# Kernel tuning notes

Measured on AMD Instinct MI355X. Metric: run time of the kernel, lower is better.

Reference implementation:

```python
import jax, jax.numpy as jnp
import numpy as np

H = 32        # query heads
KV = 8        # kv heads
HD = 128      # head_dim
EPS = 1e-6
THETA = 1e6
T = 2048
D = 4096


def _rms_norm(x, w):
    # x: [T, heads, HD]
    var = jnp.mean(jnp.square(x), axis=-1, keepdims=True)
    return x * jax.lax.rsqrt(var + EPS) * w


def _rope(x, cos, sin):
    # NEOX-style rotary: split last dim in halves. x: [T, heads, HD]
    x1, x2 = jnp.split(x, 2, axis=-1)
    return jnp.concatenate([x1 * cos - x2 * sin, x2 * cos + x1 * sin], axis=-1)


def setup_inputs() -> dict:
    key = jax.random.key(0)
    k1, k2, k3 = jax.random.split(key, 3)
    s = 1.0 / np.sqrt(D)
    return {
        "positions": jnp.arange(T, dtype=jnp.int32),
        "hidden_states": jax.random.normal(k1, (T, D), dtype=jnp.float32),
        "w_qkv": jax.random.normal(k2, (D, (H + 2 * KV) * HD), dtype=jnp.float32) * s,
        "q_norm_w": jnp.ones((HD,), dtype=jnp.float32),
        "k_norm_w": jnp.ones((HD,), dtype=jnp.float32),
        "w_o": jax.random.normal(k3, (H * HD, D), dtype=jnp.float32) * s,
    }


def reference(positions, hidden_states, w_qkv, q_norm_w, k_norm_w, w_o):
    scale = HD ** -0.5
    qkv = hidden_states @ w_qkv                              # [T, (H+2KV)*HD]
    q = qkv[:, : H * HD].reshape(T, H, HD)
    k = qkv[:, H * HD : (H + KV) * HD].reshape(T, KV, HD)
    v = qkv[:, (H + KV) * HD :].reshape(T, KV, HD)

    # per-head RMSNorm on q/k (Qwen3 QK-norm)
    q = _rms_norm(q, q_norm_w)
    k = _rms_norm(k, k_norm_w)

    # RoPE
    inv_freq = 1.0 / (THETA ** (jnp.arange(0, HD, 2, dtype=jnp.float32) / HD))
    freqs = positions.astype(jnp.float32)[:, None] * inv_freq  # [T, HD/2]
    cos = jnp.cos(freqs)[:, None, :]                            # [T, 1, HD/2]
    sin = jnp.sin(freqs)[:, None, :]
    q = _rope(q, cos, sin)
    k = _rope(k, cos, sin)

    # GQA: repeat kv heads
    rep = H // KV
    k = jnp.repeat(k, rep, axis=1)                           # [T, H, HD]
    v = jnp.repeat(v, rep, axis=1)

    # causal SDPA
    scores = jnp.einsum("thd,shd->hts", q, k) * scale        # [H, T, T]
    causal = jnp.tril(jnp.ones((T, T), dtype=bool))
    scores = jnp.where(causal[None], scores, jnp.finfo(scores.dtype).min)
    probs = jax.nn.softmax(scores, axis=-1)
    attn = jnp.einsum("hts,shd->thd", probs, v).reshape(T, H * HD)

    return attn @ w_o                                        # [T, D]
```

## Files before the change

### kernel.cpp

```cpp
#include <hip/hip_runtime.h>

#define TT   2048
#define DD   4096
#define NH   32
#define NKVH 8
#define HDM  128
#define KD   4096
#define NQKV 6144

typedef unsigned short u16;
typedef short v8s __attribute__((ext_vector_type(8)));
typedef float v4f __attribute__((ext_vector_type(4)));

#define QSCALE 0.12751744547734565f
#define EOFF   17.312340490667562f

__device__ __forceinline__ u16 f2bf(float f) {
    unsigned u = __builtin_bit_cast(unsigned, f);
    u += 0x7fffu + ((u >> 16) & 1u);
    return (u16)(u >> 16);
}
__device__ __forceinline__ float bf2f(u16 h) {
    return __builtin_bit_cast(float, ((unsigned)h) << 16);
}
__device__ __forceinline__ void gl2lds16(const void* g, void* l) {
    using gv = const __attribute__((address_space(1))) void;
    using lv = __attribute__((address_space(3))) void;
    __builtin_amdgcn_global_load_lds((gv*)g, (lv*)l, 16, 0, 0);
}

__device__ __forceinline__ void transpose_tile64(const float* __restrict__ in,
                                                 u16* __restrict__ out,
                                                 int K, int N, int n0, int k0,
                                                 float* tile, int t) {
    int rc = t >> 4, cc = (t & 15) * 4;
#pragma unroll
    for (int p = 0; p < 4; ++p) {
        int k = p * 16 + rc;
        float4 v = *(const float4*)&in[(size_t)(k0 + k) * N + n0 + cc];
        tile[k * 65 + cc] = v.x; tile[k * 65 + cc + 1] = v.y;
        tile[k * 65 + cc + 2] = v.z; tile[k * 65 + cc + 3] = v.w;
    }
    __syncthreads();
    int rn = t >> 3, ck = (t & 7) * 8;
#pragma unroll
    for (int p = 0; p < 2; ++p) {
        int n = p * 32 + rn;
        v8s tv;
#pragma unroll
        for (int j = 0; j < 8; ++j) tv[j] = (short)f2bf(tile[(ck + j) * 65 + n]);
        *(v8s*)&out[(size_t)(n0 + n) * K + k0 + ck] = tv;
    }
}

__global__ __launch_bounds__(256) void prep_all_kernel(const float* __restrict__ hidden,
                                                       u16* __restrict__ hid_bf,
                                                       const int* __restrict__ positions,
                                                       float* __restrict__ cosT,
                                                       float* __restrict__ sinT,
                                                       const float* __restrict__ w_qkv,
                                                       u16* __restrict__ wqkv_t) {
    __shared__ float tile[64 * 65];
    int b = blockIdx.x;
    if (b < 4096) {
        size_t i = ((size_t)b * 256 + threadIdx.x) * 8;
        float4 a = *(const float4*)&hidden[i];
        float4 c = *(const float4*)&hidden[i + 4];
        v8s tv;
        tv[0] = (short)f2bf(a.x); tv[1] = (short)f2bf(a.y);
        tv[2] = (short)f2bf(a.z); tv[3] = (short)f2bf(a.w);
        tv[4] = (short)f2bf(c.x); tv[5] = (short)f2bf(c.y);
        tv[6] = (short)f2bf(c.z); tv[7] = (short)f2bf(c.w);
        *(v8s*)&hid_bf[i] = tv;
    } else if (b < 4608) {
        int idx = (b - 4096) * 256 + threadIdx.x;
        int tp = idx >> 6, i = idx & 63;
        float invf = exp2f(-(float)i * 0.31143075889569023f);
        float f = (float)positions[tp] * invf;
        cosT[idx] = cosf(f);
        sinT[idx] = sinf(f);
    } else {
        int bx = b - 4608;
        int n0 = (bx % 96) * 64, k0 = (bx / 96) * 64;
        transpose_tile64(w_qkv, wqkv_t, 4096, NQKV, n0, k0, tile, threadIdx.x);
    }
}

__global__ __launch_bounds__(256) void gemm_bt_kernel(
    const u16* __restrict__ A, const u16* __restrict__ Bt, float* __restrict__ C, int N)
{
    __shared__ __align__(16) u16 smem[16896];
    u16* As = smem;
    u16* Bs = smem + 8192;
    int tid = threadIdx.x;
    int wave = tid >> 6, lane = tid & 63;
    int quad = lane >> 4, l15 = lane & 15;
    int lm = l15 & 7;
    int wm = wave >> 1, wn = wave & 1;
    int m0 = blockIdx.y * 128, n0 = blockIdx.x * 128;

    v4f acc[4][4];
    v4f z4 = {0.f, 0.f, 0.f, 0.f};
#pragma unroll
    for (int mi = 0; mi < 4; ++mi)
#pragma unroll
        for (int ni = 0; ni < 4; ++ni) acc[mi][ni] = z4;

    int rsub = lane >> 3;
    int cg = (lane & 7) ^ rsub;
    const u16* Ag = &A[(size_t)m0 * KD + cg * 8];
    const u16* Bg = &Bt[(size_t)n0 * KD + cg * 8];

    for (int k0 = 0; k0 < KD; k0 += 64) {
        __syncthreads();
#pragma unroll
        for (int c = 0; c < 4; ++c) {
            int ch = wave * 4 + c;
            int row = ch * 8 + rsub;
            gl2lds16(&Ag[(size_t)row * KD + k0], &As[ch * 512]);
            gl2lds16(&Bg[(size_t)row * KD + k0], &Bs[ch * 512]);
        }
        __syncthreads();
#pragma unroll
        for (int ks = 0; ks < 2; ++ks) {
            v8s af[4], bfr[4];
#pragma unroll
            for (int mi = 0; mi < 4; ++mi) {
                int ar = wm * 64 + mi * 16 + l15;
                af[mi] = *(const v8s*)&As[ar * 64 + ((((ks << 2) + quad) ^ lm) << 3)];
            }
#pragma unroll
            for (int ni = 0; ni < 4; ++ni) {
                int br = wn * 64 + ni * 16 + l15;
                bfr[ni] = *(const v8s*)&Bs[br * 64 + ((((ks << 2) + quad) ^ lm) << 3)];
            }
#pragma unroll
            for (int mi = 0; mi < 4; ++mi)
#pragma unroll
                for (int ni = 0; ni < 4; ++ni)
                    acc[mi][ni] = __builtin_amdgcn_mfma_f32_16x16x32_bf16(
                        af[mi], bfr[ni], acc[mi][ni], 0, 0, 0);
        }
    }
#pragma unroll
    for (int mi = 0; mi < 4; ++mi)
#pragma unroll
        for (int ni = 0; ni < 4; ++ni)
#pragma unroll
            for (int r = 0; r < 4; ++r)
                C[(size_t)(m0 + wm * 64 + mi * 16 + quad * 4 + r) * N +
                  (n0 + wn * 64 + ni * 16 + l15)] = acc[mi][ni][r];
}

__global__ __launch_bounds__(512, 2) void gemm256_qkv_kernel(
    const u16* __restrict__ A, const u16* __restrict__ Bt,
    const float* __restrict__ qw, const float* __restrict__ kw,
    const float* __restrict__ cosT, const float* __restrict__ sinT,
    u16* __restrict__ Qb, u16* __restrict__ Kb, u16* __restrict__ Vt)
{
    __shared__ __align__(16) char smem_raw[131072];
    u16* lds = (u16*)smem_raw;
    const int tid = threadIdx.x;
    const int wave = tid >> 6, lane = tid & 63;
    const int quad = lane >> 4, l15 = lane & 15, lm = l15 & 7;
    const int wm = wave >> 2, wn = wave & 3;
    const int m0 = blockIdx.y * 256, n0 = blockIdx.x * 256;

    v4f acc[2][2][4][2];
    v4f z4 = {0.f, 0.f, 0.f, 0.f};
#pragma unroll
    for (int a0 = 0; a0 < 2; ++a0)
#pragma unroll
        for (int b0 = 0; b0 < 2; ++b0)
#pragma unroll
            for (int mi = 0; mi < 4; ++mi)
#pragma unroll
                for (int ni = 0; ni < 2; ++ni) acc[a0][b0][mi][ni] = z4;

    const int rsub = lane >> 3;
    const int cg = (lane & 7) ^ rsub;
    const u16* Ag = &A[(size_t)m0 * KD + cg * 8];
    const u16* Bg = &Bt[(size_t)n0 * KD + cg * 8];
    const int ch0 = wave * 2;
    const int g0 = (quad ^ lm) << 3;
    const int g1 = ((4 + quad) ^ lm) << 3;

#define STAGE_A(tt, h) do { \
    int _b = ((tt) & 1) * 32768; \
    gl2lds16(&Ag[(size_t)((h) * 128 + (ch0 + 0) * 8 + rsub) * KD + (size_t)(tt) * 64], \
             &lds[_b + (h) * 8192 + (ch0 + 0) * 512]); \
    gl2lds16(&Ag[(size_t)((h) * 128 + (ch0 + 1) * 8 + rsub) * KD + (size_t)(tt) * 64], \
             &lds[_b + (h) * 8192 + (ch0 + 1) * 512]); \
  } while (0)
#define STAGE_B(tt, h) do { \
    int _b = ((tt) & 1) * 32768 + 16384; \
    gl2lds16(&Bg[(size_t)((h) * 128 + (ch0 + 0) * 8 + rsub) * KD + (size_t)(tt) * 64], \
             &lds[_b + (h) * 8192 + (ch0 + 0) * 512]); \
    gl2lds16(&Bg[(size_t)((h) * 128 + (ch0 + 1) * 8 + rsub) * KD + (size_t)(tt) * 64], \
             &lds[_b + (h) * 8192 + (ch0 + 1) * 512]); \
  } while (0)

    v8s af[4][2], bfr[2][2];

#define PHASE(QM, QN, RDA, RDB, STAGE_CODE, WAIT_CODE) do { \
    if (RDA) { \
      _Pragma("unroll") \
      for (int mi = 0; mi < 4; ++mi) { \
        const u16* ap = &lds[bo + ((QM) * 128 + wm * 64 + mi * 16 + l15) * 64]; \
        af[mi][0] = *(const v8s*)&ap[g0]; \
        af[mi][1] = *(const v8s*)&ap[g1]; \
      } } \
    if (RDB) { \
      _Pragma("unroll") \
      for (int ni = 0; ni < 2; ++ni) { \
        const u16* bp = &lds[bo + 16384 + ((QN) * 128 + wn * 32 + ni * 16 + l15) * 64]; \
        bfr[ni][0] = *(const v8s*)&bp[g0]; \
        bfr[ni][1] = *(const v8s*)&bp[g1]; \
      } } \
    STAGE_CODE; \
    __builtin_amdgcn_s_barrier(); \
    asm volatile("s_waitcnt lgkmcnt(0)" ::: "memory"); \
    __builtin_amdgcn_sched_barrier(0); \
    __builtin_amdgcn_s_setprio(1); \
    _Pragma("unroll") \
    for (int mi = 0; mi < 4; ++mi) \
      _Pragma("unroll") \
      for (int ni = 0; ni < 2; ++ni) { \
        acc[QM][QN][mi][ni] = __builtin_amdgcn_mfma_f32_16x16x32_bf16( \
            af[mi][0], bfr[ni][0], acc[QM][QN][mi][ni], 0, 0, 0); \
        acc[QM][QN][mi][ni] = __builtin_amdgcn_mfma_f32_16x16x32_bf16( \
            af[mi][1], bfr[ni][1], acc[QM][QN][mi][ni], 0, 0, 0); \
      } \
    __builtin_amdgcn_s_setprio(0); \
    WAIT_CODE; \
    __builtin_amdgcn_s_barrier(); \
  } while (0)

    STAGE_A(0, 0); STAGE_B(0, 0); STAGE_B(0, 1); STAGE_A(0, 1);
    STAGE_A(1, 0); STAGE_B(1, 1); STAGE_A(1, 1);
    asm volatile("s_waitcnt vmcnt(6)" ::: "memory");
    __builtin_amdgcn_s_barrier();

#pragma unroll 2
    for (int t = 0; t < 64; ++t) {
        const int bo = (t & 1) * 32768;
        PHASE(0, 0, 1, 1, { if (t + 1 < 64) STAGE_B(t + 1, 0); }, {});
        PHASE(0, 1, 0, 1, { if (t + 2 < 64) STAGE_A(t + 2, 0); }, {});
        PHASE(1, 1, 1, 0, { if (t + 2 < 64) STAGE_B(t + 2, 1); }, {});
        PHASE(1, 0, 0, 1, { if (t + 2 < 64) STAGE_A(t + 2, 1); },
              { if (t + 2 < 64) { asm volatile("s_waitcnt vmcnt(6)" ::: "memory"); }
                else            { asm volatile("s_waitcnt vmcnt(0)" ::: "memory"); } });
    }
#undef PHASE
#undef STAGE_A
#undef STAGE_B

    u16* Ct = lds;
    const int t0q = blockIdx.y * 256;
#pragma unroll
    for (int hh = 0; hh < 2; ++hh) {
        __syncthreads();
#pragma unroll
        for (int qm = 0; qm < 2; ++qm)
#pragma unroll
            for (int mi = 0; mi < 4; ++mi)
#pragma unroll
                for (int ni = 0; ni < 2; ++ni)
#pragma unroll
                    for (int r = 0; r < 4; ++r)
                        Ct[(qm * 128 + wm * 64 + mi * 16 + quad * 4 + r) * 132 +
                           wn * 32 + ni * 16 + l15] = f2bf(acc[qm][hh][mi][ni][r]);
        __syncthreads();
        const int head = blockIdx.x * 2 + hh;
        if (head < 40) {
            if (tid < 256) {
                const int row = tid;
                const float* w = (head < 32) ? qw : kw;
                float ss = 0.f;
                for (int i = 0; i < 128; ++i) {
                    float x = bf2f(Ct[row * 132 + i]);
                    ss += x * x;
                }
                float rs = rsqrtf(ss * (1.0f / 128.0f) + 1e-6f);
                if (head < 32) rs *= QSCALE;
                const int ti = t0q + row;
                for (int i = 0; i < 64; ++i) {
                    float x1 = bf2f(Ct[row * 132 + i]) * rs * w[i];
                    float x2 = bf2f(Ct[row * 132 + 64 + i]) * rs * w[64 + i];
                    float c = cosT[ti * 64 + i], s = sinT[ti * 64 + i];
                    Ct[row * 132 + i]      = f2bf(x1 * c - x2 * s);
                    Ct[row * 132 + 64 + i] = f2bf(x2 * c + x1 * s);
                }
            }
            __syncthreads();
            u16* dst = (head < 32) ? &Qb[((size_t)head * TT + t0q) * HDM]
                                   : &Kb[((size_t)(head - 32) * TT + t0q) * HDM];
            for (int cix = tid; cix < 256 * 16; cix += 512) {
                int row = cix >> 4, part = (cix & 15) * 8;
                v8s tv;
#pragma unroll
                for (int j = 0; j < 8; ++j) tv[j] = (short)Ct[row * 132 + part + j];
                *(v8s*)&dst[row * HDM + part] = tv;
            }
        } else {
            const int kvh = head - 40;
            if (tid < 128) {
                const int hd = tid;
                for (int tb = 0; tb < 32; ++tb) {
                    v8s tv;
#pragma unroll
                    for (int j = 0; j < 8; ++j) tv[j] = (short)Ct[(tb * 8 + j) * 132 + hd];
                    *(v8s*)&Vt[((size_t)kvh * HDM + hd) * TT + t0q + tb * 8] = tv;
                }
            }
        }
    }
}

__global__ __launch_bounds__(256) void attn_plus_kernel(
    const u16* __restrict__ Qb, const u16* __restrict__ Kb,
    const u16* __restrict__ Vt, u16* __restrict__ Ob,
    const float* __restrict__ w_o, u16* __restrict__ wo_t)
{
    __shared__ __align__(16) char smem_raw[40960];
    int tid = threadIdx.x;
    if (blockIdx.x >= 1024) {
        int bx = blockIdx.x - 1024;
        int n0 = (bx & 63) * 64, k0 = (bx >> 6) * 64;
        transpose_tile64(w_o, wo_t, 4096, 4096, n0, k0, (float*)smem_raw, tid);
        return;
    }
    u16* Kl = (u16*)smem_raw;
    u16* Vl = (u16*)(smem_raw + 16384);
    u16* Pl = (u16*)(smem_raw + 32768);
    int wave = tid >> 6, lane = tid & 63;
    int quad = lane >> 4, l15 = lane & 15;
    int idx = blockIdx.x;
    int h = idx & 31;
    int qb = 31 - (idx >> 5);
    int kv = h >> 2;
    int q0 = qb * 64;
    int lm = l15 & 7;

    v8s qf[4];
    {
        const u16* qr = &Qb[((size_t)h * TT + q0 + wave * 16 + l15) * HDM];
#pragma unroll
        for (int ks = 0; ks < 4; ++ks) qf[ks] = *(const v8s*)&qr[ks * 32 + quad * 8];
    }

    v4f z4 = {0.f, 0.f, 0.f, 0.f};
    v4f of[8];
#pragma unroll
    for (int i = 0; i < 8; ++i) of[i] = z4;
    float lsum[4];
#pragma unroll
    for (int r = 0; r < 4; ++r) lsum[r] = 0.f;
    u16* Pw = &Pl[wave * 1024];

    for (int s0 = 0; s0 <= q0; s0 += 64) {
        __syncthreads();
#pragma unroll
        for (int c = 0; c < 4; ++c) {
            int ch = wave * 4 + c;
            int rk = ch * 4 + (lane >> 4);
            int ck = (lane & 15) ^ (rk & 7);
            gl2lds16(&Kb[((size_t)kv * TT + s0 + rk) * HDM + ck * 8], &Kl[ch * 512]);
            int rv = ch * 8 + (lane >> 3);
            int cv = (lane & 7) ^ (rv & 7);
            gl2lds16(&Vt[((size_t)kv * HDM + rv) * TT + s0 + cv * 8], &Vl[ch * 512]);
        }
        __syncthreads();
        v4f sf[4];
#pragma unroll
        for (int nt = 0; nt < 4; ++nt) {
            v4f cacc = z4;
#pragma unroll
            for (int ks = 0; ks < 4; ++ks)
                cacc = __builtin_amdgcn_mfma_f32_16x16x32_bf16(
                    qf[ks],
                    *(const v8s*)&Kl[(nt * 16 + l15) * 128 + (((ks * 4 + quad) ^ lm) << 3)],
                    cacc, 0, 0, 0);
            sf[nt] = cacc;
        }
        if (s0 == q0) {
#pragma unroll
            for (int nt = 0; nt < 4; ++nt) {
                int sg = s0 + nt * 16 + l15;
#pragma unroll
                for (int r = 0; r < 4; ++r) {
                    int qg = q0 + wave * 16 + quad * 4 + r;
                    if (sg > qg) sf[nt][r] = -3.0e38f;
                }
            }
        }
#pragma unroll
        for (int nt = 0; nt < 4; ++nt)
#pragma unroll
            for (int r = 0; r < 4; ++r) {
                float p = exp2f(sf[nt][r] - EOFF);
                sf[nt][r] = p;
                lsum[r] += p;
            }
#pragma unroll
        for (int nt = 0; nt < 4; ++nt)
#pragma unroll
            for (int r = 0; r < 4; ++r) {
                int row = quad * 4 + r;
                int pch = ((nt << 1) + (l15 >> 3)) ^ (row & 7);
                Pw[row * 64 + pch * 8 + (l15 & 7)] = f2bf(sf[nt][r]);
            }
#pragma unroll
        for (int sub = 0; sub < 2; ++sub) {
            v8s pa = *(const v8s*)&Pw[l15 * 64 + ((((sub << 2) + quad) ^ lm) << 3)];
#pragma unroll
            for (int nt = 0; nt < 8; ++nt)
                of[nt] = __builtin_amdgcn_mfma_f32_16x16x32_bf16(
                    pa,
                    *(const v8s*)&Vl[(nt * 16 + l15) * 64 + ((((sub << 2) + quad) ^ lm) << 3)],
                    of[nt], 0, 0, 0);
        }
    }
#pragma unroll
    for (int off = 1; off < 16; off <<= 1)
#pragma unroll
        for (int r = 0; r < 4; ++r) lsum[r] += __shfl_xor(lsum[r], off, 64);
    float invl[4];
#pragma unroll
    for (int r = 0; r < 4; ++r) invl[r] = 1.0f / lsum[r];
#pragma unroll
    for (int nt = 0; nt < 8; ++nt)
#pragma unroll
        for (int r = 0; r < 4; ++r)
            Ob[(size_t)(q0 + wave * 16 + quad * 4 + r) * (NH * HDM) + h * HDM + nt * 16 + l15] =
                f2bf(of[nt][r] * invl[r]);
}

extern "C" void kernel_launch(void* const* d_in, const int* in_sizes, int n_in,
                              void* d_out, int out_size, void* d_ws, size_t ws_size,
                              hipStream_t stream)
{
    (void)in_sizes; (void)n_in; (void)out_size; (void)ws_size;
    const int*   positions = (const int*)d_in[0];
    const float* hidden    = (const float*)d_in[1];
    const float* w_qkv     = (const float*)d_in[2];
    const float* q_norm_w  = (const float*)d_in[3];
    const float* k_norm_w  = (const float*)d_in[4];
    const float* w_o       = (const float*)d_in[5];
    float* out = (float*)d_out;
    char* ws = (char*)d_ws;
    char* ob = (char*)d_out;

    u16* hid_bf = (u16*)(ws + 0);
    u16* attnO  = (u16*)(ws + 0);
    u16* wqkv_t = (u16*)(ws + (size_t)16777216);
    u16* wo_t   = (u16*)(ws + (size_t)16777216);

    u16*   Qb   = (u16*)(ob + 0);
    u16*   Kb   = (u16*)(ob + (size_t)16777216);
    u16*   Vt   = (u16*)(ob + (size_t)20971520);
    float* cosT = (float*)(ob + (size_t)25165824);
    float* sinT = (float*)(ob + (size_t)25690112);

    prep_all_kernel<<<10752, 256, 0, stream>>>(hidden, hid_bf, positions, cosT, sinT,
                                               w_qkv, wqkv_t);

    gemm256_qkv_kernel<<<dim3(24, 8), 512, 0, stream>>>(
        hid_bf, wqkv_t, q_norm_w, k_norm_w, cosT, sinT, Qb, Kb, Vt);

    attn_plus_kernel<<<5120, 256, 0, stream>>>(Qb, Kb, Vt, attnO, w_o, wo_t);

    gemm_bt_kernel<<<dim3(32, 16), 256, 0, stream>>>(attnO, wo_t, out, 4096);
}
```

Baseline: 484.4 us.

## Manually unroll GEMM main loop with constant buffer offsets and reordered MFMA k-steps

Replaces the runtime-indexed double-buffer loop with an explicit two-iteration body using compile-time LDS offsets, peeling the tail so stage guards disappear. MFMAs are reordered to consume the first k-half of all fragments before the second, and a partial lgkmcnt wait is inserted so MFMAs can start while later LDS reads complete. This aims to cut address arithmetic, branch overhead, and LDS-read latency exposure, at the cost of larger code size and reliance on correct waitcnt counts.

```diff
diff --git a/kernel.cpp b/kernel.cpp
--- a/kernel.cpp
+++ b/kernel.cpp
@@ -202,58 +202,74 @@
 
     v8s af[4][2], bfr[2][2];
 
-#define PHASE(QM, QN, RDA, RDB, STAGE_CODE, WAIT_CODE) do { \
+#define PHASE(BO, QM, QN, RDA, RDB, PRE, STAGE_CODE, WAIT_CODE) do { \
     if (RDA) { \
       _Pragma("unroll") \
       for (int mi = 0; mi < 4; ++mi) { \
-        const u16* ap = &lds[bo + ((QM) * 128 + wm * 64 + mi * 16 + l15) * 64]; \
+        const u16* ap = &lds[(BO) + ((QM) * 128 + wm * 64 + mi * 16 + l15) * 64]; \
         af[mi][0] = *(const v8s*)&ap[g0]; \
         af[mi][1] = *(const v8s*)&ap[g1]; \
       } } \
     if (RDB) { \
       _Pragma("unroll") \
       for (int ni = 0; ni < 2; ++ni) { \
-        const u16* bp = &lds[bo + 16384 + ((QN) * 128 + wn * 32 + ni * 16 + l15) * 64]; \
+        const u16* bp = &lds[(BO) + 16384 + ((QN) * 128 + wn * 32 + ni * 16 + l15) * 64]; \
         bfr[ni][0] = *(const v8s*)&bp[g0]; \
         bfr[ni][1] = *(const v8s*)&bp[g1]; \
       } } \
     STAGE_CODE; \
+    PRE; \
     __builtin_amdgcn_s_barrier(); \
     asm volatile("s_waitcnt lgkmcnt(0)" ::: "memory"); \
     __builtin_amdgcn_sched_barrier(0); \
     __builtin_amdgcn_s_setprio(1); \
     _Pragma("unroll") \
-    for (int mi = 0; mi < 4; ++mi) \
+    for (int ks = 0; ks < 2; ++ks) \
       _Pragma("unroll") \
-      for (int ni = 0; ni < 2; ++ni) { \
-        acc[QM][QN][mi][ni] = __builtin_amdgcn_mfma_f32_16x16x32_bf16( \
-            af[mi][0], bfr[ni][0], acc[QM][QN][mi][ni], 0, 0, 0); \
-        acc[QM][QN][mi][ni] = __builtin_amdgcn_mfma_f32_16x16x32_bf16( \
-            af[mi][1], bfr[ni][1], acc[QM][QN][mi][ni], 0, 0, 0); \
-      } \
+      for (int mi = 0; mi < 4; ++mi) \
+        _Pragma("unroll") \
+        for (int ni = 0; ni < 2; ++ni) \
+          acc[QM][QN][mi][ni] = __builtin_amdgcn_mfma_f32_16x16x32_bf16( \
+              af[mi][ks], bfr[ni][ks], acc[QM][QN][mi][ni], 0, 0, 0); \
     __builtin_amdgcn_s_setprio(0); \
     WAIT_CODE; \
     __builtin_amdgcn_s_barrier(); \
   } while (0)
 
+#define PRE1 asm volatile("s_waitcnt lgkmcnt(8)" ::: "memory")
+#define VM6  asm volatile("s_waitcnt vmcnt(6)" ::: "memory")
+#define VM0  asm volatile("s_waitcnt vmcnt(0)" ::: "memory")
+
     STAGE_A(0, 0); STAGE_B(0, 0); STAGE_B(0, 1); STAGE_A(0, 1);
     STAGE_A(1, 0); STAGE_B(1, 1); STAGE_A(1, 1);
-    asm volatile("s_waitcnt vmcnt(6)" ::: "memory");
+    VM6;
     __builtin_amdgcn_s_barrier();
 
-#pragma unroll 2
-    for (int t = 0; t < 64; ++t) {
-        const int bo = (t & 1) * 32768;
-        PHASE(0, 0, 1, 1, { if (t + 1 < 64) STAGE_B(t + 1, 0); }, {});
-        PHASE(0, 1, 0, 1, { if (t + 2 < 64) STAGE_A(t + 2, 0); }, {});
-        PHASE(1, 1, 1, 0, { if (t + 2 < 64) STAGE_B(t + 2, 1); }, {});
-        PHASE(1, 0, 0, 1, { if (t + 2 < 64) STAGE_A(t + 2, 1); },
-              { if (t + 2 < 64) { asm volatile("s_waitcnt vmcnt(6)" ::: "memory"); }
-                else            { asm volatile("s_waitcnt vmcnt(0)" ::: "memory"); } });
-    }
+    for (int u = 0; u < 31; ++u) {
+        const int t = 2 * u;
+        PHASE(0, 0, 0, 1, 1, PRE1, STAGE_B(t + 1, 0), {});
+        PHASE(0, 0, 1, 0, 1, {},   STAGE_A(t + 2, 0), {});
+        PHASE(0, 1, 1, 1, 0, {},   STAGE_B(t + 2, 1), {});
+        PHASE(0, 1, 0, 0, 1, {},   STAGE_A(t + 2, 1), VM6);
+        PHASE(32768, 0, 0, 1, 1, PRE1, STAGE_B(t + 2, 0), {});
+        PHASE(32768, 0, 1, 0, 1, {},   STAGE_A(t + 3, 0), {});
+        PHASE(32768, 1, 1, 1, 0, {},   STAGE_B(t + 3, 1), {});
+        PHASE(32768, 1, 0, 0, 1, {},   STAGE_A(t + 3, 1), VM6);
+    }
+    PHASE(0, 0, 0, 1, 1, PRE1, STAGE_B(63, 0), {});
+    PHASE(0, 0, 1, 0, 1, {}, {}, {});
+    PHASE(0, 1, 1, 1, 0, {}, {}, {});
+    PHASE(0, 1, 0, 0, 1, {}, {}, VM0);
+    PHASE(32768, 0, 0, 1, 1, PRE1, {}, {});
+    PHASE(32768, 0, 1, 0, 1, {}, {}, {});
+    PHASE(32768, 1, 1, 1, 0, {}, {}, {});
+    PHASE(32768, 1, 0, 0, 1, {}, {}, {});
 #undef PHASE
 #undef STAGE_A
 #undef STAGE_B
+#undef PRE1
+#undef VM6
+#undef VM0
 
     u16* Ct = lds;
     const int t0q = blockIdx.y * 256;
```

Result: no change. 478.0 us (-1.3%).
